# Optimization experiments

Hardware: AMD Instinct MI355X
Metric: run time of the kernel (lower is better)

The kernel has to match this reference:

```python
import jax, jax.numpy as jnp
import numpy as np

# Hyperparameters (from HOIMLoss init_kwargs / defaults)
NUM_PIDS = 5532
NUM_CQ = 5000
NUM_BG = 5000
NUM_FEATURES = 256
BATCH = 4096
OIM_SCALAR = 30.0
ALPHA_D = 0.25
ALPHA_R = 0.25
GAMMA_D = 2.0
GAMMA_R = 2.0


def _l2norm(x):
    return x / jnp.maximum(jnp.linalg.norm(x, axis=-1, keepdims=True), 1e-12)


def setup_inputs() -> dict:
    key = jax.random.key(0)
    k1, k2, k3, k4, k5 = jax.random.split(key, 5)
    inputs = _l2norm(jax.random.normal(k1, (BATCH, NUM_FEATURES), dtype=jnp.float32))
    # roi_label: -2 = background, -1 = ignored unlabeled, [0, NUM_PIDS) = identity
    roi_label = jax.random.randint(k2, (BATCH,), -2, NUM_PIDS)
    lut = _l2norm(jax.random.normal(k3, (NUM_PIDS, NUM_FEATURES), dtype=jnp.float32))
    cq = _l2norm(jax.random.normal(k4, (NUM_CQ, NUM_FEATURES), dtype=jnp.float32))
    cqb = _l2norm(jax.random.normal(k5, (NUM_BG, NUM_FEATURES), dtype=jnp.float32))
    return {"inputs": inputs, "roi_label": roi_label, "lut": lut, "cq": cq, "cqb": cqb}


def reference(inputs, roi_label, lut, cq, cqb):
    # OIM2CQ.forward: concat([inputs@cqb.T, inputs@lut.T, inputs@cq.T], dim=1)
    table = jnp.concatenate([cqb, lut, cq], axis=0)        # [BG+P+CQ, F]
    projected = OIM_SCALAR * (inputs @ table.T)            # [B, BG+P+CQ]

    valid = roi_label >= -1      # non-background rows (inds in torch code)
    labeled = roi_label >= 0     # rows contributing to nll (ignore_index=-1)

    # OIM focal loss over non-background columns [labeled | unlabeled]
    proj_non_bg = projected[:, NUM_BG:]                    # [B, P+CQ]
    logp = jax.nn.log_softmax(proj_non_bg, axis=-1)
    p = jnp.exp(logp)
    focal_p = ALPHA_R * (1.0 - p) ** GAMMA_R * logp
    safe_lab = jnp.clip(roi_label, 0, NUM_PIDS - 1)
    row_loss = -jnp.take_along_axis(focal_p, safe_lab[:, None], axis=1)[:, 0]
    row_loss = jnp.where(labeled, row_loss, 0.0)           # ignore_index=-1 -> 0

    # Detection focal loss over (background, foreground) mass
    all_probs = jax.nn.softmax(projected, axis=-1)
    cls_score = jnp.stack(
        [all_probs[:, :NUM_BG].sum(axis=-1), all_probs[:, NUM_BG:].sum(axis=-1)],
        axis=-1,
    )                                                      # [B, 2]
    det_label = jnp.clip(roi_label + 2, 0, 1)              # -2 -> 0, else 1
    focal_det = ALPHA_D * (1.0 - cls_score) ** GAMMA_D * jnp.log(cls_score)
    loss_det = -jnp.take_along_axis(focal_det, det_label[:, None], axis=1)[:, 0].mean()

    # dynamic_lambda: weight per-row oim loss by detached fg prob squared
    cls_non_bg = jax.lax.stop_gradient(cls_score[:, 1])
    row_loss = row_loss * cls_non_bg ** 2
    n_valid = jnp.maximum(valid.sum(), 1).astype(projected.dtype)
    loss_oim = jnp.sum(jnp.where(valid, row_loss, 0.0)) / n_valid

    return cls_score, loss_det, loss_oim
```

## Files before the change

### kernel.cpp

```cpp
#include <hip/hip_runtime.h>
#include <hip/hip_bf16.h>

typedef unsigned short u16;
typedef unsigned int u32;
typedef __attribute__((ext_vector_type(8))) short bf16x8;
typedef __attribute__((ext_vector_type(4))) short bf16x4;
typedef __attribute__((ext_vector_type(4))) float f32x4;

#define NBG   5000
#define NPID  5532
#define NTOT  15532
#define FEAT  256
#define BATCH 4096
#define SCALE_LOG2E 43.280851226668994f
#define LPITCH 264

#define NTILE_B  976
#define TILE_SH  4096
#define NTILE_A  256

#define TABT_BYTES ((size_t)NTILE_B * TILE_SH * 2)
#define AT_BYTES   ((size_t)NTILE_A * TILE_SH * 2)
#define SUMS_OFF   (TABT_BYTES + AT_BYTES)
#define SUMS_FLOATS 8196
#define WS_NEED    (SUMS_OFF + SUMS_FLOATS * 4)

__device__ __forceinline__ void atomic_add_f(float* p, float v) {
    __hip_atomic_fetch_add(p, v, __ATOMIC_RELAXED, __HIP_MEMORY_SCOPE_AGENT);
}
__device__ __forceinline__ float atomic_ld_f(const float* p) {
    return __hip_atomic_load(p, __ATOMIC_RELAXED, __HIP_MEMORY_SCOPE_AGENT);
}
__device__ __forceinline__ short f2bf(float f) {
    return (short)__bfloat16_as_ushort(__float2bfloat16(f));
}
__device__ __forceinline__ float bf2f(u16 u) {
    union { u32 i; float f; } v; v.i = ((u32)u) << 16; return v.f;
}

__device__ __forceinline__ const float* table_row(
    int n, const float* __restrict__ lut, const float* __restrict__ cq,
    const float* __restrict__ cqb)
{
    const int nc = n < NTOT ? n : NTOT - 1;
    if (nc < NBG)        return cqb + (size_t)nc * FEAT;
    if (nc < NBG + NPID) return lut + (size_t)(nc - NBG) * FEAT;
    return cq + (size_t)(nc - NBG - NPID) * FEAT;
}

#define PRE_BLOCKS (NTILE_B + NTILE_A)

__global__ __launch_bounds__(256) void prepass_kernel(
    const float* __restrict__ inputs, const float* __restrict__ lut,
    const float* __restrict__ cq, const float* __restrict__ cqb,
    u16* __restrict__ tabt, u16* __restrict__ at, float* __restrict__ S)
{
    __shared__ __align__(16) short tl[TILE_SH];
    const int b = blockIdx.x, tid = threadIdx.x;
    const int fid = b * 256 + tid;
    if (fid < SUMS_FLOATS) S[fid] = 0.f;

    const bool isA = (b >= NTILE_B);
    const int tile = isA ? (b - NTILE_B) : b;
    u16* dst = (isA ? at : tabt) + (size_t)tile * TILE_SH;

    const int row = tid >> 4;
    const int c16 = tid & 15;
    bool ok = true;
    const float* src;
    if (isA) {
        src = inputs + (size_t)(tile * 16 + row) * FEAT + c16 * 16;
    } else {
        const int cg = tile * 16 + row;
        ok = cg < NTOT;
        src = table_row(cg, lut, cq, cqb) + c16 * 16;
    }
    #pragma unroll
    for (int i = 0; i < 4; ++i) {
        const f32x4 v = *(const f32x4*)(src + i * 4);
        const int P = c16 * 16 + i * 4;
        const int kk = P >> 5, q = (P >> 3) & 3, sub = P & 7;
        const bf16x4 h = ok ? bf16x4{ f2bf(v[0]), f2bf(v[1]), f2bf(v[2]), f2bf(v[3]) }
                            : bf16x4{ 0, 0, 0, 0 };
        *(bf16x4*)(tl + kk * 512 + q * 128 + row * 8 + sub) = h;
    }
    __syncthreads();
    *(bf16x8*)(dst + tid * 8)        = *(const bf16x8*)(tl + tid * 8);
    *(bf16x8*)(dst + 2048 + tid * 8) = *(const bf16x8*)(tl + 2048 + tid * 8);
}

__global__ __launch_bounds__(256, 2) void score_bf16_kernel(
    const u16* __restrict__ tabt, const u16* __restrict__ at,
    float* __restrict__ sum_bg, float* __restrict__ sum_nb)
{
    __shared__ __align__(16) short lbuf0[TILE_SH];
    __shared__ __align__(16) short lbuf1[TILE_SH];

    const int lid = blockIdx.x;
    const int x8  = lid & 7;
    const int j   = lid >> 3;
    const int rowchunk = x8 * 2 + (j & 1);
    const int colchunk = j >> 1;

    const int tid  = threadIdx.x;
    const int wave = tid >> 6;
    const int lane = tid & 63;
    const int l15  = lane & 15;
    const int quad = lane >> 4;

    bf16x8 af[4][8];
    {
        const u16* ab = at + (size_t)(rowchunk * 16 + wave * 4) * TILE_SH
                           + quad * 128 + l15 * 8;
        #pragma unroll
        for (int s = 0; s < 4; ++s)
            #pragma unroll
            for (int kk = 0; kk < 8; ++kk)
                af[s][kk] = *(const bf16x8*)(ab + (size_t)s * TILE_SH + kk * 512);
    }

    float pbg[16], pnb[16];
    #pragma unroll
    for (int i = 0; i < 16; ++i) { pbg[i] = 0.f; pnb[i] = 0.f; }

    const int bt0  = colchunk * 16;
    const int tmax = (colchunk == 60) ? 12 : 16;

    auto loadg = [&](int bt, bf16x8& a, bf16x8& b) {
        const u16* g = tabt + (size_t)bt * TILE_SH;
        a = *(const bf16x8*)(g + tid * 8);
        b = *(const bf16x8*)(g + 2048 + tid * 8);
    };
    auto consume = [&](const short* lb, int bt) {
        f32x4 cc[4];
        #pragma unroll
        for (int s = 0; s < 4; ++s) cc[s] = f32x4{0.f, 0.f, 0.f, 0.f};
        #pragma unroll
        for (int kk = 0; kk < 8; ++kk) {
            const bf16x8 b = *(const bf16x8*)(lb + kk * 512 + quad * 128 + l15 * 8);
            cc[0] = __builtin_amdgcn_mfma_f32_16x16x32_bf16(af[0][kk], b, cc[0], 0, 0, 0);
            cc[1] = __builtin_amdgcn_mfma_f32_16x16x32_bf16(af[1][kk], b, cc[1], 0, 0, 0);
            cc[2] = __builtin_amdgcn_mfma_f32_16x16x32_bf16(af[2][kk], b, cc[2], 0, 0, 0);
            cc[3] = __builtin_amdgcn_mfma_f32_16x16x32_bf16(af[3][kk], b, cc[3], 0, 0, 0);
        }
        if (colchunk != 60) {
            if (bt < 312) {
                #pragma unroll
                for (int s = 0; s < 4; ++s)
                    #pragma unroll
                    for (int r = 0; r < 4; ++r)
                        pbg[s * 4 + r] += exp2f(cc[s][r] * SCALE_LOG2E);
            } else if (bt > 312) {
                #pragma unroll
                for (int s = 0; s < 4; ++s)
                    #pragma unroll
                    for (int r = 0; r < 4; ++r)
                        pnb[s * 4 + r] += exp2f(cc[s][r] * SCALE_LOG2E);
            } else {
                const bool isbg = l15 < 8;
                #pragma unroll
                for (int s = 0; s < 4; ++s)
                    #pragma unroll
                    for (int r = 0; r < 4; ++r) {
                        const float e = exp2f(cc[s][r] * SCALE_LOG2E);
                        pbg[s * 4 + r] += isbg ? e : 0.f;
                        pnb[s * 4 + r] += isbg ? 0.f : e;
                    }
            }
        } else {
            const bool okc = (bt * 16 + l15) < NTOT;
            #pragma unroll
            for (int s = 0; s < 4; ++s)
                #pragma unroll
                for (int r = 0; r < 4; ++r) {
                    const float e = exp2f(cc[s][r] * SCALE_LOG2E);
                    pnb[s * 4 + r] += okc ? e : 0.f;
                }
        }
    };

    bf16x8 r0, r1;
    loadg(bt0, r0, r1);

    #pragma unroll 1
    for (int tp = 0; tp < tmax; tp += 2) {
        *(bf16x8*)(lbuf0 + tid * 8) = r0;
        *(bf16x8*)(lbuf0 + 2048 + tid * 8) = r1;
        __syncthreads();
        if (tp + 1 < tmax) loadg(bt0 + tp + 1, r0, r1);
        consume(lbuf0, bt0 + tp);

        *(bf16x8*)(lbuf1 + tid * 8) = r0;
        *(bf16x8*)(lbuf1 + 2048 + tid * 8) = r1;
        __syncthreads();
        if (tp + 2 < tmax) loadg(bt0 + tp + 2, r0, r1);
        consume(lbuf1, bt0 + tp + 1);
    }

    #pragma unroll
    for (int off = 1; off < 16; off <<= 1) {
        #pragma unroll
        for (int i = 0; i < 16; ++i) {
            pbg[i] += __shfl_xor(pbg[i], off);
            pnb[i] += __shfl_xor(pnb[i], off);
        }
    }
    if (l15 == 0) {
        #pragma unroll
        for (int s = 0; s < 4; ++s) {
            #pragma unroll
            for (int r = 0; r < 4; ++r) {
                const int row = (rowchunk * 16 + wave * 4 + s) * 16 + quad * 4 + r;
                atomic_add_f(&sum_bg[row], pbg[s * 4 + r]);
                atomic_add_f(&sum_nb[row], pnb[s * 4 + r]);
            }
        }
    }
}

__global__ __launch_bounds__(256, 2) void score_f32_kernel(
    const float* __restrict__ inputs, const float* __restrict__ lut,
    const float* __restrict__ cq, const float* __restrict__ cqb,
    float* __restrict__ sum_bg, float* __restrict__ sum_nb)
{
    __shared__ __align__(16) short lds[32 * LPITCH];
    const int wave = threadIdx.x >> 6;
    const int lane = threadIdx.x & 63;
    const int l15  = lane & 15;
    const int quad = lane >> 4;
    const int rowbase = blockIdx.y * 256;
    const int colbase = blockIdx.x * 256;

    bf16x8 afrag[4][8];
    #pragma unroll 1
    for (int c = 0; c < 8; ++c) {
        __syncthreads();
        #pragma unroll
        for (int i = 0; i < 8; ++i) {
            const int lr = i * 4 + wave;
            const f32x4 v = *(const f32x4*)(inputs + (size_t)(rowbase + c * 32 + lr) * FEAT + lane * 4);
            bf16x4 h = { f2bf(v[0]), f2bf(v[1]), f2bf(v[2]), f2bf(v[3]) };
            *(bf16x4*)(&lds[lr * LPITCH + lane * 4]) = h;
        }
        __syncthreads();
        if ((c >> 1) == wave) {
            const int half = c & 1;
            #pragma unroll
            for (int j2 = 0; j2 < 2; ++j2) {
                const int lr = j2 * 16 + l15;
                #pragma unroll
                for (int kk = 0; kk < 8; ++kk)
                    afrag[half * 2 + j2][kk] =
                        *(const bf16x8*)(&lds[lr * LPITCH + kk * 32 + quad * 8]);
            }
        }
    }

    float pbg[16], pnb[16];
    #pragma unroll
    for (int i = 0; i < 16; ++i) { pbg[i] = 0.f; pnb[i] = 0.f; }

    #pragma unroll 1
    for (int s = 0; s < 8; ++s) {
        __syncthreads();
        #pragma unroll
        for (int i = 0; i < 8; ++i) {
            const int lc = i * 4 + wave;
            const f32x4 v = *(const f32x4*)(table_row(colbase + s * 32 + lc, lut, cq, cqb) + lane * 4);
            bf16x4 h = { f2bf(v[0]), f2bf(v[1]), f2bf(v[2]), f2bf(v[3]) };
            *(bf16x4*)(&lds[lc * LPITCH + lane * 4]) = h;
        }
        __syncthreads();

        #pragma unroll
        for (int st = 0; st < 2; ++st) {
            const int lc = st * 16 + l15;
            f32x4 cc[4];
            #pragma unroll
            for (int q = 0; q < 4; ++q) cc[q] = f32x4{0.f, 0.f, 0.f, 0.f};
            #pragma unroll
            for (int kk = 0; kk < 8; ++kk) {
                const bf16x8 b = *(const bf16x8*)(&lds[lc * LPITCH + kk * 32 + quad * 8]);
                cc[0] = __builtin_amdgcn_mfma_f32_16x16x32_bf16(afrag[0][kk], b, cc[0], 0, 0, 0);
                cc[1] = __builtin_amdgcn_mfma_f32_16x16x32_bf16(afrag[1][kk], b, cc[1], 0, 0, 0);
                cc[2] = __builtin_amdgcn_mfma_f32_16x16x32_bf16(afrag[2][kk], b, cc[2], 0, 0, 0);
                cc[3] = __builtin_amdgcn_mfma_f32_16x16x32_bf16(afrag[3][kk], b, cc[3], 0, 0, 0);
            }
            const int n = colbase + s * 32 + st * 16 + l15;
            const bool okc  = n < NTOT;
            const bool isbg = n < NBG;
            #pragma unroll
            for (int q = 0; q < 4; ++q) {
                #pragma unroll
                for (int r = 0; r < 4; ++r) {
                    float e = exp2f(cc[q][r] * SCALE_LOG2E);
                    e = okc ? e : 0.f;
                    pbg[q * 4 + r] += isbg ? e : 0.f;
                    pnb[q * 4 + r] += isbg ? 0.f : e;
                }
            }
        }
    }

    #pragma unroll
    for (int off = 1; off < 16; off <<= 1) {
        #pragma unroll
        for (int i = 0; i < 16; ++i) {
            pbg[i] += __shfl_xor(pbg[i], off);
            pnb[i] += __shfl_xor(pnb[i], off);
        }
    }
    if (l15 == 0) {
        #pragma unroll
        for (int q = 0; q < 4; ++q) {
            #pragma unroll
            for (int r = 0; r < 4; ++r) {
                const int row = rowbase + wave * 64 + q * 16 + quad * 4 + r;
                atomic_add_f(&sum_bg[row], pbg[q * 4 + r]);
                atomic_add_f(&sum_nb[row], pnb[q * 4 + r]);
            }
        }
    }
}

__global__ __launch_bounds__(256) void finalize_kernel(
    const float* __restrict__ inputs, const int* __restrict__ roi_label,
    const float* __restrict__ lut,
    const float* __restrict__ sum_bg, const float* __restrict__ sum_nb,
    float* __restrict__ accums, unsigned int* __restrict__ ticket,
    float* __restrict__ out)
{
    __shared__ float s_det[4], s_oim[4], s_nv[4];
    const int wid  = threadIdx.x >> 6;
    const int lane = threadIdx.x & 63;

    float det_a = 0.f, oim_a = 0.f, nv_a = 0.f;

    #pragma unroll 1
    for (int it = 0; it < 8; ++it) {
        const int row = blockIdx.x * 32 + wid * 8 + it;
        const int r   = roi_label[row];

        float dot = 0.f;
        {
            const int rc = r < 0 ? 0 : r;
            const f32x4 xi = *(const f32x4*)(inputs + (size_t)row * FEAT + lane * 4);
            const f32x4 li = *(const f32x4*)(lut + (size_t)rc * FEAT + lane * 4);
            #pragma unroll
            for (int jj = 0; jj < 4; ++jj)
                dot += bf2f((u16)f2bf(xi[jj])) * bf2f((u16)f2bf(li[jj]));
        }
        #pragma unroll
        for (int off = 32; off > 0; off >>= 1) dot += __shfl_xor(dot, off);

        if (lane == 0) {
            const float sbg = sum_bg[row];
            const float snb = sum_nb[row];
            const float inv = 1.f / (sbg + snb);
            const float cls0 = sbg * inv;
            const float cls1 = snb * inv;
            out[2 * row]     = cls0;
            out[2 * row + 1] = cls1;

            const float cs = (r >= -1) ? cls1 : cls0;
            const float om = 1.f - cs;
            det_a += -(0.25f * om * om * logf(cs)) * (1.f / (float)BATCH);
            nv_a  += (r >= -1) ? 1.f : 0.f;

            if (r >= 0) {
                const float logp = 30.f * dot - logf(snb);
                const float p    = expf(logp);
                const float om2  = 1.f - p;
                oim_a += -(0.25f * om2 * om2 * logp) * cls1 * cls1;
            }
        }
    }

    if (lane == 0) { s_det[wid] = det_a; s_oim[wid] = oim_a; s_nv[wid] = nv_a; }
    __syncthreads();
    if (threadIdx.x == 0) {
        atomic_add_f(&accums[0], s_det[0] + s_det[1] + s_det[2] + s_det[3]);
        atomic_add_f(&accums[1], s_oim[0] + s_oim[1] + s_oim[2] + s_oim[3]);
        atomic_add_f(&accums[2], s_nv[0] + s_nv[1] + s_nv[2] + s_nv[3]);
        __threadfence();
        const unsigned t = __hip_atomic_fetch_add(ticket, 1u, __ATOMIC_ACQ_REL,
                                                  __HIP_MEMORY_SCOPE_AGENT);
        if (t == gridDim.x - 1) {
            const float det = atomic_ld_f(&accums[0]);
            const float oim = atomic_ld_f(&accums[1]);
            float nv        = atomic_ld_f(&accums[2]);
            if (nv < 1.f) nv = 1.f;
            out[2 * BATCH]     = det;
            out[2 * BATCH + 1] = oim / nv;
        }
    }
}

extern "C" void kernel_launch(void* const* d_in, const int* in_sizes, int n_in,
                              void* d_out, int out_size, void* d_ws, size_t ws_size,
                              hipStream_t stream)
{
    const float* inputs = (const float*)d_in[0];
    const int*   roi    = (const int*)d_in[1];
    const float* lut    = (const float*)d_in[2];
    const float* cq     = (const float*)d_in[3];
    const float* cqb    = (const float*)d_in[4];
    float* out = (float*)d_out;

    if (ws_size >= (size_t)WS_NEED) {
        u16* tabt = (u16*)d_ws;
        u16* at   = (u16*)((char*)d_ws + TABT_BYTES);
        float* S  = (float*)((char*)d_ws + SUMS_OFF);
        prepass_kernel<<<PRE_BLOCKS, 256, 0, stream>>>(inputs, lut, cq, cqb, tabt, at, S);
        score_bf16_kernel<<<976, 256, 0, stream>>>(tabt, at, S, S + BATCH);
        finalize_kernel<<<128, 256, 0, stream>>>(
            inputs, roi, lut, S, S + BATCH, S + 2 * BATCH,
            (unsigned int*)(S + 2 * BATCH + 3), out);
    } else {
        float* S = (float*)d_ws;
        hipMemsetAsync(S, 0, SUMS_FLOATS * sizeof(float), stream);
        dim3 g1(61, 16);
        score_f32_kernel<<<g1, 256, 0, stream>>>(inputs, lut, cq, cqb, S, S + BATCH);
        finalize_kernel<<<128, 256, 0, stream>>>(
            inputs, roi, lut, S, S + BATCH, S + 2 * BATCH,
            (unsigned int*)(S + 2 * BATCH + 3), out);
    }
}
```

Baseline: 154.0 us.

## Stage two table tiles per barrier and raise score kernel occupancy bound

```diff
diff --git a/kernel.cpp b/kernel.cpp
--- a/kernel.cpp
+++ b/kernel.cpp
@@ -89,12 +89,14 @@
     *(bf16x8*)(dst + 2048 + tid * 8) = *(const bf16x8*)(tl + 2048 + tid * 8);
 }
 
-__global__ __launch_bounds__(256, 2) void score_bf16_kernel(
+__global__ __launch_bounds__(256, 4) void score_bf16_kernel(
     const u16* __restrict__ tabt, const u16* __restrict__ at,
     float* __restrict__ sum_bg, float* __restrict__ sum_nb)
 {
-    __shared__ __align__(16) short lbuf0[TILE_SH];
-    __shared__ __align__(16) short lbuf1[TILE_SH];
+    __shared__ __align__(16) short lbA0[TILE_SH];
+    __shared__ __align__(16) short lbA1[TILE_SH];
+    __shared__ __align__(16) short lbB0[TILE_SH];
+    __shared__ __align__(16) short lbB1[TILE_SH];
 
     const int lid = blockIdx.x;
     const int x8  = lid & 7;
@@ -123,8 +125,8 @@
     #pragma unroll
     for (int i = 0; i < 16; ++i) { pbg[i] = 0.f; pnb[i] = 0.f; }
 
-    const int bt0  = colchunk * 16;
-    const int tmax = (colchunk == 60) ? 12 : 16;
+    const int bt0 = colchunk * 16;
+    const int nph = (colchunk == 60) ? 6 : 8;
 
     auto loadg = [&](int bt, bf16x8& a, bf16x8& b) {
         const u16* g = tabt + (size_t)bt * TILE_SH;
@@ -179,22 +181,25 @@
         }
     };
 
-    bf16x8 r0, r1;
-    loadg(bt0, r0, r1);
+    bf16x8 ra0, ra1, rb0, rb1;
+    loadg(bt0, ra0, ra1);
+    loadg(bt0 + 1, rb0, rb1);
 
     #pragma unroll 1
-    for (int tp = 0; tp < tmax; tp += 2) {
-        *(bf16x8*)(lbuf0 + tid * 8) = r0;
-        *(bf16x8*)(lbuf0 + 2048 + tid * 8) = r1;
+    for (int ph = 0; ph < nph; ++ph) {
+        short* w0 = (ph & 1) ? lbB0 : lbA0;
+        short* w1 = (ph & 1) ? lbB1 : lbA1;
+        *(bf16x8*)(w0 + tid * 8) = ra0;
+        *(bf16x8*)(w0 + 2048 + tid * 8) = ra1;
+        *(bf16x8*)(w1 + tid * 8) = rb0;
+        *(bf16x8*)(w1 + 2048 + tid * 8) = rb1;
         __syncthreads();
-        if (tp + 1 < tmax) loadg(bt0 + tp + 1, r0, r1);
-        consume(lbuf0, bt0 + tp);
-
-        *(bf16x8*)(lbuf1 + tid * 8) = r0;
-        *(bf16x8*)(lbuf1 + 2048 + tid * 8) = r1;
-        __syncthreads();
-        if (tp + 2 < tmax) loadg(bt0 + tp + 2, r0, r1);
-        consume(lbuf1, bt0 + tp + 1);
+        if (ph + 1 < nph) {
+            loadg(bt0 + 2 * ph + 2, ra0, ra1);
+            loadg(bt0 + 2 * ph + 3, rb0, rb1);
+        }
+        consume(w0, bt0 + 2 * ph);
+        consume(w1, bt0 + 2 * ph + 1);
     }
 
     #pragma unroll
```

Result: slower. 398.1 us (+158.5%).
